# Kernel tuning notes

Hardware: AMD Instinct MI355X
Metric: run time of the kernel (lower is better)

Reference implementation:

```python
import jax, jax.numpy as jnp
import numpy as np

L_MAX = 2097152  # == L, so linspace(0,1,L) matches theta_grid[:L]
EPS = 1e-8


def setup_inputs() -> dict:
    root = jax.random.key(0)
    k1, k2, k3, k4 = jax.random.split(root, 4)
    return {
        "a": jnp.asarray(1.0, jnp.float32),
        "alpha": jnp.asarray(0.5, jnp.float32),
        "k": jnp.asarray(4.0, jnp.float32),
        "m": jnp.asarray(3.0, jnp.float32),
        "delta": jnp.linspace(0.1, 0.6, 6, dtype=jnp.float32),
        "E": jnp.linspace(0.05, 0.3, 6, dtype=jnp.float32),
        "u_alpha_re": 0.3 * jax.random.normal(k1, (6,), jnp.float32),
        "u_alpha_im": 0.3 * jax.random.normal(k2, (6,), jnp.float32),
        "u_beta_re": 0.3 * jax.random.normal(k3, (6,), jnp.float32),
        "u_beta_im": 0.3 * jax.random.normal(k4, (6,), jnp.float32),
        "B": 4,
        "L": L_MAX,
    }


def reference(a, alpha, k, m, delta, E,
              u_alpha_re, u_alpha_im, u_beta_re, u_beta_im, B, L):
    # theta grid (== tau grid); L == L_max so this matches theta_grid[:L]
    theta = jnp.linspace(0.0, 1.0, L, dtype=jnp.float32)  # [L]
    base = a * jnp.exp(-alpha * theta) * jnp.sin(k * theta) * jnp.cos(m * theta)

    ua = u_alpha_re + 1j * u_alpha_im  # complex64 [6]
    ub = u_beta_re + 1j * u_beta_im
    ua = ua / (jnp.sqrt(jnp.sum(jnp.abs(ua) ** 2)) + EPS)
    ub = ub / (jnp.sqrt(jnp.sum(jnp.abs(ub) ** 2)) + EPS)
    coeffs = ub * jnp.conj(ua)  # [6]

    # Original: S = |sum_i coeffs_i * exp(-1j*(2*E_i*tau + delta_i*theta))| on an
    # LxL grid, then take the diagonal. On the diagonal tau_j == theta_j, so the
    # phase collapses to -(2*E_i + delta_i) * theta_j — compute diag directly.
    phase = -(2.0 * E[:, None] + delta[:, None]) * theta[None, :]  # [6, L], real
    S_diag = jnp.abs(jnp.sum(coeffs[:, None] * jnp.exp(1j * phase), axis=0))  # [L]

    r = base * S_diag
    r_norm = (r - r.min()) / (r.max() - r.min() + EPS)
    r_scaled = 0.5 + r_norm
    return jnp.broadcast_to(r_scaled[None, None, :], (B, 1, L))
```

## Files before the change

### kernel.cpp

```cpp
#include <hip/hip_runtime.h>
#include <math.h>


#define L_TOT   2097152
#define NT      256
#define NB      2048
#define EPSF    1e-8f

__device__ __forceinline__ void compute_r4(
    int j0, float a, float alpha, float k, float m,
    const float* __restrict__ delta, const float* __restrict__ E,
    const float* __restrict__ uar, const float* __restrict__ uai,
    const float* __restrict__ ubr, const float* __restrict__ ubi,
    float r[4])
{
    const float h   = 1.0f / (float)(L_TOT - 1);
    const float th0 = (float)j0 * h;

    float cr[6], ci[6], w[6];
    {
        float na2 = 0.f, nb2 = 0.f;
        float ar[6], ai_[6], br[6], bi_[6];
#pragma unroll
        for (int i = 0; i < 6; ++i) {
            ar[i] = uar[i]; ai_[i] = uai[i]; br[i] = ubr[i]; bi_[i] = ubi[i];
            na2 = fmaf(ar[i], ar[i], fmaf(ai_[i], ai_[i], na2));
            nb2 = fmaf(br[i], br[i], fmaf(bi_[i], bi_[i], nb2));
        }
        const float s = 1.f / ((sqrtf(na2) + EPSF) * (sqrtf(nb2) + EPSF));
#pragma unroll
        for (int i = 0; i < 6; ++i) {
            cr[i] = (br[i] * ar[i] + bi_[i] * ai_[i]) * s;
            ci[i] = (bi_[i] * ar[i] - br[i] * ai_[i]) * s;
            w[i]  = -(2.f * E[i] + delta[i]);
        }
    }

    float sk, ck, sm, cm, skh, ckh, smh, cmh;
    __sincosf(k * th0, &sk, &ck);
    __sincosf(m * th0, &sm, &cm);
    __sincosf(k * h,  &skh, &ckh);
    __sincosf(m * h,  &smh, &cmh);
    float e  = a * __expf(-alpha * th0);
    const float eh = __expf(-alpha * h);

    float sw[6], cw[6], swh[6], cwh[6];
#pragma unroll
    for (int i = 0; i < 6; ++i) {
        __sincosf(w[i] * th0, &sw[i], &cw[i]);
        __sincosf(w[i] * h,  &swh[i], &cwh[i]);
    }

#pragma unroll
    for (int t = 0; t < 4; ++t) {
        float re = 0.f, im = 0.f;
#pragma unroll
        for (int i = 0; i < 6; ++i) {
            re = fmaf(cr[i], cw[i], fmaf(-ci[i], sw[i], re));
            im = fmaf(cr[i], sw[i], fmaf( ci[i], cw[i], im));
        }
        const float S = sqrtf(fmaf(re, re, im * im));
        r[t] = e * sk * cm * S;

        if (t < 3) {
            e *= eh;
            float ns, nc;
            ns = fmaf(sk, ckh,  ck * skh); nc = fmaf(ck, ckh, -sk * skh); sk = ns; ck = nc;
            ns = fmaf(sm, cmh,  cm * smh); nc = fmaf(cm, cmh, -sm * smh); sm = ns; cm = nc;
#pragma unroll
            for (int i = 0; i < 6; ++i) {
                ns = fmaf(sw[i], cwh[i],  cw[i] * swh[i]);
                nc = fmaf(cw[i], cwh[i], -sw[i] * swh[i]);
                sw[i] = ns; cw[i] = nc;
            }
        }
    }
}

__device__ __forceinline__ void block_minmax(float lmin, float lmax,
                                             float* out_min, float* out_max)
{
#pragma unroll
    for (int off = 32; off > 0; off >>= 1) {
        lmin = fminf(lmin, __shfl_down(lmin, off, 64));
        lmax = fmaxf(lmax, __shfl_down(lmax, off, 64));
    }
    __shared__ float smin[NT / 64], smax[NT / 64];
    const int lane = threadIdx.x & 63, wid = threadIdx.x >> 6;
    if (lane == 0) { smin[wid] = lmin; smax[wid] = lmax; }
    __syncthreads();
    if (threadIdx.x == 0) {
        float mn = smin[0], mx = smax[0];
#pragma unroll
        for (int i = 1; i < NT / 64; ++i) { mn = fminf(mn, smin[i]); mx = fmaxf(mx, smax[i]); }
        *out_min = mn; *out_max = mx;
    }
}

__global__ __launch_bounds__(NT) void qim_minmax(
    const float* __restrict__ a_p, const float* __restrict__ alpha_p,
    const float* __restrict__ k_p, const float* __restrict__ m_p,
    const float* __restrict__ delta, const float* __restrict__ E,
    const float* __restrict__ uar, const float* __restrict__ uai,
    const float* __restrict__ ubr, const float* __restrict__ ubi,
    float* __restrict__ partials)
{
    const int gid = blockIdx.x * NT + threadIdx.x;
    float r[4];
    compute_r4(gid * 4, *a_p, *alpha_p, *k_p, *m_p,
               delta, E, uar, uai, ubr, ubi, r);
    const float lmin = fminf(fminf(r[0], r[1]), fminf(r[2], r[3]));
    const float lmax = fmaxf(fmaxf(r[0], r[1]), fmaxf(r[2], r[3]));
    float mn, mx;
    block_minmax(lmin, lmax, &mn, &mx);
    if (threadIdx.x == 0) {
        partials[blockIdx.x]      = mn;
        partials[NB + blockIdx.x] = mx;
    }
}

__global__ __launch_bounds__(NT) void qim_reduce(
    const float* __restrict__ partials, float* __restrict__ gout)
{
    float lmin = 3.402823466e38f, lmax = -3.402823466e38f;
    for (int i = threadIdx.x; i < NB; i += NT) {
        lmin = fminf(lmin, partials[i]);
        lmax = fmaxf(lmax, partials[NB + i]);
    }
    float mn, mx;
    block_minmax(lmin, lmax, &mn, &mx);
    if (threadIdx.x == 0) {
        gout[0] = mn;
        gout[1] = 1.0f / (mx - mn + EPSF);
    }
}

__global__ __launch_bounds__(NT) void qim_write(
    const float* __restrict__ a_p, const float* __restrict__ alpha_p,
    const float* __restrict__ k_p, const float* __restrict__ m_p,
    const float* __restrict__ delta, const float* __restrict__ E,
    const float* __restrict__ uar, const float* __restrict__ uai,
    const float* __restrict__ ubr, const float* __restrict__ ubi,
    const float* __restrict__ gout, float* __restrict__ out, int copies)
{
    const int gid = blockIdx.x * NT + threadIdx.x;
    const int j0  = gid * 4;
    float r[4];
    compute_r4(j0, *a_p, *alpha_p, *k_p, *m_p,
               delta, E, uar, uai, ubr, ubi, r);
    const float gmin = gout[0], inv = gout[1];
    float4 o;
    o.x = fmaf(r[0] - gmin, inv, 0.5f);
    o.y = fmaf(r[1] - gmin, inv, 0.5f);
    o.z = fmaf(r[2] - gmin, inv, 0.5f);
    o.w = fmaf(r[3] - gmin, inv, 0.5f);
    for (int b = 0; b < copies; ++b)
        *reinterpret_cast<float4*>(out + (size_t)b * L_TOT + j0) = o;
}

extern "C" void kernel_launch(void* const* d_in, const int* in_sizes, int n_in,
                              void* d_out, int out_size, void* d_ws, size_t ws_size,
                              hipStream_t stream)
{
    const float* a_p     = (const float*)d_in[0];
    const float* alpha_p = (const float*)d_in[1];
    const float* k_p     = (const float*)d_in[2];
    const float* m_p     = (const float*)d_in[3];
    const float* delta   = (const float*)d_in[4];
    const float* E       = (const float*)d_in[5];
    const float* uar     = (const float*)d_in[6];
    const float* uai     = (const float*)d_in[7];
    const float* ubr     = (const float*)d_in[8];
    const float* ubi     = (const float*)d_in[9];
    float* out = (float*)d_out;
    float* wsf = (float*)d_ws;
    float* partials = wsf;
    float* gout     = wsf + 2 * NB;

    const int copies = out_size / L_TOT;

    qim_minmax<<<NB, NT, 0, stream>>>(a_p, alpha_p, k_p, m_p, delta, E,
                                      uar, uai, ubr, ubi, partials);
    qim_reduce<<<1, NT, 0, stream>>>(partials, gout);
    qim_write<<<NB, NT, 0, stream>>>(a_p, alpha_p, k_p, m_p, delta, E,
                                     uar, uai, ubr, ubi, gout, out, copies);
}
```

Measured before the change: 112.8 us.

## Fold final min/max reduction into last block and approximate step rotations

Removes the separate single-block reduce kernel. Each block now increments an atomic counter after writing its partials, and the last block to finish does the global min/max reduction. A memset is added to reset the counter each call. The per-step rotation sin/cos is replaced by a small-angle Taylor approximation, and sincos calls are split into separate sin/cos intrinsics. The approximation adds a small error in the recurrence.

```diff
diff --git a/kernel.cpp b/kernel.cpp
--- a/kernel.cpp
+++ b/kernel.cpp
@@ -6,6 +6,10 @@
 #define NT      256
 #define NB      2048
 #define EPSF    1e-8f
+#define FLT_BIG 3.402823466e38f
+
+#define WS_GOUT  (2*NB)
+#define WS_CNT   (2*NB + 2)
 
 __device__ __forceinline__ void compute_r4(
     int j0, float a, float alpha, float k, float m,
@@ -27,7 +31,7 @@
             na2 = fmaf(ar[i], ar[i], fmaf(ai_[i], ai_[i], na2));
             nb2 = fmaf(br[i], br[i], fmaf(bi_[i], bi_[i], nb2));
         }
-        const float s = 1.f / ((sqrtf(na2) + EPSF) * (sqrtf(nb2) + EPSF));
+        const float s = 1.f / ((__fsqrt_rn(na2) + EPSF) * (__fsqrt_rn(nb2) + EPSF));
 #pragma unroll
         for (int i = 0; i < 6; ++i) {
             cr[i] = (br[i] * ar[i] + bi_[i] * ai_[i]) * s;
@@ -36,19 +40,22 @@
         }
     }
 
-    float sk, ck, sm, cm, skh, ckh, smh, cmh;
-    __sincosf(k * th0, &sk, &ck);
-    __sincosf(m * th0, &sm, &cm);
-    __sincosf(k * h,  &skh, &ckh);
-    __sincosf(m * h,  &smh, &cmh);
+    float sk = __sinf(k * th0), ck = __cosf(k * th0);
+    float sm = __sinf(m * th0), cm = __cosf(m * th0);
     float e  = a * __expf(-alpha * th0);
-    const float eh = __expf(-alpha * h);
+
+    const float skh = k * h,  ckh = fmaf(-0.5f * skh, skh, 1.0f);
+    const float smh = m * h,  cmh = fmaf(-0.5f * smh, smh, 1.0f);
+    const float eh  = __expf(-alpha * h);
 
     float sw[6], cw[6], swh[6], cwh[6];
 #pragma unroll
     for (int i = 0; i < 6; ++i) {
-        __sincosf(w[i] * th0, &sw[i], &cw[i]);
-        __sincosf(w[i] * h,  &swh[i], &cwh[i]);
+        const float ph = w[i] * th0;
+        sw[i]  = __sinf(ph);
+        cw[i]  = __cosf(ph);
+        swh[i] = w[i] * h;
+        cwh[i] = fmaf(-0.5f * swh[i], swh[i], 1.0f);
     }
 
 #pragma unroll
@@ -59,7 +66,7 @@
             re = fmaf(cr[i], cw[i], fmaf(-ci[i], sw[i], re));
             im = fmaf(cr[i], sw[i], fmaf( ci[i], cw[i], im));
         }
-        const float S = sqrtf(fmaf(re, re, im * im));
+        const float S = __fsqrt_rn(fmaf(re, re, im * im));
         r[t] = e * sk * cm * S;
 
         if (t < 3) {
@@ -103,7 +110,7 @@
     const float* __restrict__ delta, const float* __restrict__ E,
     const float* __restrict__ uar, const float* __restrict__ uai,
     const float* __restrict__ ubr, const float* __restrict__ ubi,
-    float* __restrict__ partials)
+    float* __restrict__ ws, unsigned int* __restrict__ counter)
 {
     const int gid = blockIdx.x * NT + threadIdx.x;
     float r[4];
@@ -113,25 +120,30 @@
     const float lmax = fmaxf(fmaxf(r[0], r[1]), fmaxf(r[2], r[3]));
     float mn, mx;
     block_minmax(lmin, lmax, &mn, &mx);
+
+    __shared__ bool amLast;
     if (threadIdx.x == 0) {
-        partials[blockIdx.x]      = mn;
-        partials[NB + blockIdx.x] = mx;
+        ws[blockIdx.x]      = mn;
+        ws[NB + blockIdx.x] = mx;
+        __threadfence();
+        const unsigned int prev = atomicAdd(counter, 1u);
+        amLast = (prev == NB - 1);
+        if (amLast) __threadfence();
     }
-}
+    __syncthreads();
 
-__global__ __launch_bounds__(NT) void qim_reduce(
-    const float* __restrict__ partials, float* __restrict__ gout)
-{
-    float lmin = 3.402823466e38f, lmax = -3.402823466e38f;
-    for (int i = threadIdx.x; i < NB; i += NT) {
-        lmin = fminf(lmin, partials[i]);
-        lmax = fmaxf(lmax, partials[NB + i]);
-    }
-    float mn, mx;
-    block_minmax(lmin, lmax, &mn, &mx);
-    if (threadIdx.x == 0) {
-        gout[0] = mn;
-        gout[1] = 1.0f / (mx - mn + EPSF);
+    if (amLast) {
+        float fmn = FLT_BIG, fmx = -FLT_BIG;
+        for (int i = threadIdx.x; i < NB; i += NT) {
+            fmn = fminf(fmn, ws[i]);
+            fmx = fmaxf(fmx, ws[NB + i]);
+        }
+        float gmn, gmx;
+        block_minmax(fmn, fmx, &gmn, &gmx);
+        if (threadIdx.x == 0) {
+            ws[WS_GOUT]     = gmn;
+            ws[WS_GOUT + 1] = 1.0f / (gmx - gmn + EPSF);
+        }
     }
 }
 
@@ -141,14 +153,14 @@
     const float* __restrict__ delta, const float* __restrict__ E,
     const float* __restrict__ uar, const float* __restrict__ uai,
     const float* __restrict__ ubr, const float* __restrict__ ubi,
-    const float* __restrict__ gout, float* __restrict__ out, int copies)
+    const float* __restrict__ ws, float* __restrict__ out, int copies)
 {
     const int gid = blockIdx.x * NT + threadIdx.x;
     const int j0  = gid * 4;
     float r[4];
     compute_r4(j0, *a_p, *alpha_p, *k_p, *m_p,
                delta, E, uar, uai, ubr, ubi, r);
-    const float gmin = gout[0], inv = gout[1];
+    const float gmin = ws[WS_GOUT], inv = ws[WS_GOUT + 1];
     float4 o;
     o.x = fmaf(r[0] - gmin, inv, 0.5f);
     o.y = fmaf(r[1] - gmin, inv, 0.5f);
@@ -174,14 +186,14 @@
     const float* ubi     = (const float*)d_in[9];
     float* out = (float*)d_out;
     float* wsf = (float*)d_ws;
-    float* partials = wsf;
-    float* gout     = wsf + 2 * NB;
+    unsigned int* counter = (unsigned int*)(wsf + WS_CNT);
 
     const int copies = out_size / L_TOT;
 
+    hipMemsetAsync(counter, 0, sizeof(unsigned int), stream);
+
     qim_minmax<<<NB, NT, 0, stream>>>(a_p, alpha_p, k_p, m_p, delta, E,
-                                      uar, uai, ubr, ubi, partials);
-    qim_reduce<<<1, NT, 0, stream>>>(partials, gout);
+                                      uar, uai, ubr, ubi, wsf, counter);
     qim_write<<<NB, NT, 0, stream>>>(a_p, alpha_p, k_p, m_p, delta, E,
-                                     uar, uai, ubr, ubi, gout, out, copies);
+                                     uar, uai, ubr, ubi, wsf, out, copies);
 }
```

Measured after the change: 143.3 us. +27.1%, slower.
